# Performance work log

Hardware: AMD Instinct MI355X
Metric: run time of the kernel (lower is better)

The kernel has to match this reference:

```python
import jax, jax.numpy as jnp
import numpy as np

NUM_EXPERT = 64
TOP_K = 2
N_TOKENS = 16384
H_DIM = 4096


def setup_inputs() -> dict:
    key = jax.random.key(0)
    k1, k2, k3 = jax.random.split(key, 3)
    x = jax.random.normal(k1, (N_TOKENS, H_DIM), dtype=jnp.float32)
    # nn.Linear(h_dim, num_expert): weight [E, H], bias [E]
    W = jax.random.normal(k2, (NUM_EXPERT, H_DIM), dtype=jnp.float32) * (1.0 / np.sqrt(H_DIM))
    b = jax.random.normal(k3, (NUM_EXPERT,), dtype=jnp.float32) * 0.01
    return {"x": x, "W": W, "b": b}


def reference(x, W, b):
    # gating linear: [N, H] @ [H, E] + [E] -> [N, E]
    router_logits = x @ W.T + b
    # softmax over experts in float32 (matches dtype=torch.float)
    router_probs = jax.nn.softmax(router_logits.astype(jnp.float32), axis=1)
    # top-k over experts (values sorted descending, like torch.topk)
    router_weights, selected_experts_idx = jax.lax.top_k(router_probs, TOP_K)
    # renormalize via second softmax over the top_k dim (dim=1 of [N, K])
    router_weights = jax.nn.softmax(router_weights, axis=1).astype(x.dtype)
    # one-hot expert mask [N, K, E] -> permute(2,1,0) -> [E, K, N]
    expert_mask = jax.nn.one_hot(selected_experts_idx, NUM_EXPERT, dtype=jnp.int32)
    expert_mask = jnp.transpose(expert_mask, (2, 1, 0))
    return router_logits, router_weights, selected_experts_idx, expert_mask
```

## Files before the change

### kernel.cpp

```cpp
#include <hip/hip_runtime.h>
#include <hip/hip_bf16.h>
#include <math.h>

#define H_DIM 4096
#define N_EXP 64
#define N_TOK 16384
#define BM    32
#define KB    64
#define NCHUNK (H_DIM / KB)
#define MARGIN 1e-3f
#define SLOT_BYTES 24576

typedef __attribute__((ext_vector_type(8))) short short8v;
typedef __attribute__((ext_vector_type(4))) float float4v;

__device__ __forceinline__ unsigned short bf16_rn(float f) {
    unsigned u = __builtin_bit_cast(unsigned, f);
    u += 0x7FFFu + ((u >> 16) & 1u);
    return (unsigned short)(u >> 16);
}
__device__ __forceinline__ float bf16_hi_f32(unsigned u) {
    return __builtin_bit_cast(float, u & 0xFFFF0000u);
}
__device__ __forceinline__ void gload_lds16(const void* g, void* l) {
    __builtin_amdgcn_global_load_lds(
        (const __attribute__((address_space(1))) unsigned int*)g,
        (__attribute__((address_space(3))) unsigned int*)l, 16, 0, 0);
}

__global__ __launch_bounds__(256)
void wconvert_kernel(const float* __restrict__ W,
                     unsigned short* __restrict__ wh,
                     unsigned short* __restrict__ wm,
                     int* __restrict__ counter) {
    int i = blockIdx.x * 256 + threadIdx.x;
    if (i == 0) *counter = 0;
    float w = W[i];
    unsigned u = __builtin_bit_cast(unsigned, w);
    wh[i] = (unsigned short)(u >> 16);
    wm[i] = bf16_rn(w - bf16_hi_f32(u));
}

__global__ __launch_bounds__(512, 4)
void router_mfma_kernel(const float* __restrict__ x,
                        const unsigned short* __restrict__ wh,
                        const unsigned short* __restrict__ wm,
                        const float* __restrict__ bias,
                        float* __restrict__ logits,
                        float* __restrict__ wout,
                        float* __restrict__ iout,
                        int* __restrict__ counter,
                        int* __restrict__ list) {
    __shared__ char smem[2 * SLOT_BYTES];
    float* olds = (float*)smem;

    const int tid  = threadIdx.x;
    const int lane = tid & 63;
    const int wid  = __builtin_amdgcn_readfirstlane(tid >> 6);
    const int tok0 = blockIdx.x * BM;

    const int q    = lane >> 4;
    const int e15  = lane & 15;
    const int mt   = wid & 1;
    const int eg   = wid >> 1;
    const int arow = mt * 16 + e15;
    const int er   = eg * 16 + e15;

    float4v acc = {0.f, 0.f, 0.f, 0.f};

    auto stage = [&](int slot, int kc) {
        char* base = smem + slot * SLOT_BYTES;
        {
            int row = tid >> 4, u = tid & 15;
            int us  = u ^ (row & 15);
            const float* src = x + (size_t)(tok0 + row) * H_DIM + kc + us * 4;
            gload_lds16(src, base + (size_t)(wid * 64) * 16);
        }
#pragma unroll
        for (int j = 0; j < 2; ++j) {
            int idx = j * 512 + tid;
            int s = idx >> 9, e = (idx >> 3) & 63, u = idx & 7;
            int us = u ^ (e & 7);
            const unsigned short* wsrc = s ? wm : wh;
            const unsigned short* src  = wsrc + (size_t)e * H_DIM + kc + us * 8;
            gload_lds16(src, base + 8192 + (size_t)(j * 512 + wid * 64) * 16);
        }
    };

    auto compute = [&](int slot) {
        const char* xc = smem + slot * SLOT_BYTES;
        const char* wc = xc + 8192;
#pragma unroll
        for (int t = 0; t < 2; ++t) {
            float f[8];
#pragma unroll
            for (int h = 0; h < 2; ++h) {
                int u = (t * 8 + q * 2 + h) ^ (arow & 15);
                float4 a = *(const float4*)(xc + (size_t)(arow * 16 + u) * 16);
                f[h * 4 + 0] = a.x; f[h * 4 + 1] = a.y;
                f[h * 4 + 2] = a.z; f[h * 4 + 3] = a.w;
            }
            short8v ah, am;
#pragma unroll
            for (int j = 0; j < 8; ++j) {
                unsigned u = __builtin_bit_cast(unsigned, f[j]);
                ah[j] = (short)(u >> 16);
                am[j] = (short)bf16_rn(f[j] - bf16_hi_f32(u));
            }
            int up = (t * 4 + q) ^ (e15 & 7);
            short8v bh = *(const short8v*)(wc + (size_t)(er * 8 + up) * 16);
            short8v bm = *(const short8v*)(wc + 8192 + (size_t)(er * 8 + up) * 16);

            acc = __builtin_amdgcn_mfma_f32_16x16x32_bf16(ah, bh, acc, 0, 0, 0);
            acc = __builtin_amdgcn_mfma_f32_16x16x32_bf16(am, bh, acc, 0, 0, 0);
            acc = __builtin_amdgcn_mfma_f32_16x16x32_bf16(ah, bm, acc, 0, 0, 0);
            acc = __builtin_amdgcn_mfma_f32_16x16x32_bf16(am, bm, acc, 0, 0, 0);
        }
    };

    stage(0, 0);
    for (int c = 0; c < NCHUNK; ++c) {
        __builtin_amdgcn_s_barrier();
        if (c + 1 < NCHUNK) {
            stage((c + 1) & 1, (c + 1) * KB);
            asm volatile("s_waitcnt vmcnt(3)" ::: "memory");
        } else {
            asm volatile("s_waitcnt vmcnt(0)" ::: "memory");
        }
        __builtin_amdgcn_s_barrier();
        compute(c & 1);
    }
    __syncthreads();

    float bv = bias[er];
#pragma unroll
    for (int r = 0; r < 4; ++r) {
        int trow = mt * 16 + q * 4 + r;
        float v = acc[r] + bv;
        logits[(size_t)(tok0 + trow) * N_EXP + er] = v;
        olds[trow * 66 + er] = v;
    }
    __syncthreads();

#pragma unroll
    for (int it = 0; it < 4; ++it) {
        const int nl = wid * 4 + it;
        const int n  = tok0 + nl;
        float l = olds[nl * 66 + lane];

        float v1 = l; int i1 = lane;
#pragma unroll
        for (int off = 32; off >= 1; off >>= 1) {
            float ov = __shfl_xor(v1, off);
            int   oi = __shfl_xor(i1, off);
            if (ov > v1 || (ov == v1 && oi < i1)) { v1 = ov; i1 = oi; }
        }
        float l2 = (lane == i1) ? -INFINITY : l;
        float v2 = l2; int i2 = lane;
#pragma unroll
        for (int off = 32; off >= 1; off >>= 1) {
            float ov = __shfl_xor(v2, off);
            int   oi = __shfl_xor(i2, off);
            if (ov > v2 || (ov == v2 && oi < i2)) { v2 = ov; i2 = oi; }
        }
        float l3 = (lane == i1 || lane == i2) ? -INFINITY : l;
        float v3 = l3;
#pragma unroll
        for (int off = 32; off >= 1; off >>= 1)
            v3 = fmaxf(v3, __shfl_xor(v3, off));

        float Z = expf(l - v1);
#pragma unroll
        for (int off = 32; off >= 1; off >>= 1) Z += __shfl_xor(Z, off);

        if (lane == 0) {
            float p1 = 1.0f / Z;
            float p2 = expf(v2 - v1) / Z;
            float t  = expf(p2 - p1);
            wout[2 * n + 0] = 1.0f / (1.0f + t);
            wout[2 * n + 1] = t / (1.0f + t);
            iout[2 * n + 0] = (float)i1;
            iout[2 * n + 1] = (float)i2;
            if ((v1 - v2 < MARGIN) || (v2 - v3 < MARGIN)) {
                int sidx = atomicAdd(counter, 1);
                list[sidx] = n;
            }
        }
    }
}

__global__ __launch_bounds__(256)
void router_logits_f32(const float* __restrict__ x,
                       const float* __restrict__ W,
                       const float* __restrict__ bias,
                       float* __restrict__ logits) {
    __shared__ float4 wlds[32 * 64];
    __shared__ float4 xlds[32][32];
    const int tid = threadIdx.x;
    const int lane = tid & 63;
    const int wid = __builtin_amdgcn_readfirstlane(tid >> 6);
    const int tok0b = blockIdx.x * 32;
    const int trow0 = wid * 8;
    float acc[8];
#pragma unroll
    for (int t = 0; t < 8; ++t) acc[t] = 0.0f;
    for (int kc = 0; kc < H_DIM; kc += 128) {
        __syncthreads();
#pragma unroll
        for (int i = 0; i < 8; ++i) {
            int idx = tid + i * 256;
            int se = idx >> 5, sj = idx & 31;
            float4 v = *(const float4*)(W + (size_t)se * H_DIM + kc + sj * 4);
            wlds[sj * 64 + (se ^ (sj & 7))] = v;
        }
#pragma unroll
        for (int i = 0; i < 4; ++i) {
            int idx = tid + i * 256;
            int row = idx >> 5, col = idx & 31;
            xlds[row][col] = *(const float4*)(x + (size_t)(tok0b + row) * H_DIM + kc + col * 4);
        }
        __syncthreads();
#pragma unroll 4
        for (int jg = 0; jg < 32; ++jg) {
            float4 w = wlds[jg * 64 + (lane ^ (jg & 7))];
#pragma unroll
            for (int t = 0; t < 8; ++t) {
                float4 xv = xlds[trow0 + t][jg];
                acc[t] = fmaf(w.x, xv.x, acc[t]);
                acc[t] = fmaf(w.y, xv.y, acc[t]);
                acc[t] = fmaf(w.z, xv.z, acc[t]);
                acc[t] = fmaf(w.w, xv.w, acc[t]);
            }
        }
    }
    float bv = bias[lane];
#pragma unroll
    for (int t = 0; t < 8; ++t)
        logits[(size_t)(tok0b + trow0 + t) * N_EXP + lane] = acc[t] + bv;
}

__global__ __launch_bounds__(256)
void topk_kernel(const float* __restrict__ logits,
                 float* __restrict__ wout,
                 float* __restrict__ iout) {
    const int lane = threadIdx.x & 63;
    const int wid  = threadIdx.x >> 6;
    const int wg   = blockIdx.x * 4 + wid;
#pragma unroll
    for (int it = 0; it < 4; ++it) {
        const int n = wg * 4 + it;
        float l = logits[(size_t)n * N_EXP + lane];
        float v1 = l; int i1 = lane;
#pragma unroll
        for (int off = 32; off >= 1; off >>= 1) {
            float ov = __shfl_xor(v1, off);
            int   oi = __shfl_xor(i1, off);
            if (ov > v1 || (ov == v1 && oi < i1)) { v1 = ov; i1 = oi; }
        }
        float l2 = (lane == i1) ? -INFINITY : l;
        float v2 = l2; int i2 = lane;
#pragma unroll
        for (int off = 32; off >= 1; off >>= 1) {
            float ov = __shfl_xor(v2, off);
            int   oi = __shfl_xor(i2, off);
            if (ov > v2 || (ov == v2 && oi < i2)) { v2 = ov; i2 = oi; }
        }
        float Z = expf(l - v1);
#pragma unroll
        for (int off = 32; off >= 1; off >>= 1) Z += __shfl_xor(Z, off);
        if (lane == 0) {
            float p1 = 1.0f / Z;
            float p2 = expf(v2 - v1) / Z;
            float t  = expf(p2 - p1);
            wout[2 * n + 0] = 1.0f / (1.0f + t);
            wout[2 * n + 1] = t / (1.0f + t);
            iout[2 * n + 0] = (float)i1;
            iout[2 * n + 1] = (float)i2;
        }
    }
}

__global__ __launch_bounds__(256)
void fixup_kernel(const float* __restrict__ x,
                  const float* __restrict__ W,
                  const float* __restrict__ bias,
                  float* __restrict__ wout,
                  float* __restrict__ iout,
                  const int* __restrict__ counter,
                  const int* __restrict__ list) {
    __shared__ float plds[4][64];
    __shared__ float llds[64];
    int cnt = counter[0];
    if (cnt > N_TOK) cnt = N_TOK;
    const int e = threadIdx.x & 63;
    const int s = threadIdx.x >> 6;
    for (int it = blockIdx.x; it < cnt; it += 128) {
        int n = list[it];
        const float4* xr = (const float4*)(x + (size_t)n * H_DIM) + s * 256;
        const float4* wr = (const float4*)(W + (size_t)e * H_DIM) + s * 256;
        float p = 0.f;
#pragma unroll 8
        for (int j = 0; j < 256; ++j) {
            float4 a = xr[j], w = wr[j];
            p = fmaf(a.x, w.x, p); p = fmaf(a.y, w.y, p);
            p = fmaf(a.z, w.z, p); p = fmaf(a.w, w.w, p);
        }
        plds[s][e] = p;
        __syncthreads();
        if (threadIdx.x < 64)
            llds[e] = ((plds[0][e] + plds[1][e]) + (plds[2][e] + plds[3][e])) + bias[e];
        __syncthreads();
        if (threadIdx.x == 0) {
            float v1 = -INFINITY, v2 = -INFINITY;
            int i1 = 0, i2 = 0;
            for (int i = 0; i < 64; ++i) {
                float li = llds[i];
                if (li > v1)      { v2 = v1; i2 = i1; v1 = li; i1 = i; }
                else if (li > v2) { v2 = li; i2 = i; }
            }
            float Z = 0.0f;
            for (int i = 0; i < 64; ++i) Z += expf(llds[i] - v1);
            float p1 = 1.0f / Z;
            float p2 = expf(v2 - v1) / Z;
            float t  = expf(p2 - p1);
            wout[2 * n + 0] = 1.0f / (1.0f + t);
            wout[2 * n + 1] = t / (1.0f + t);
            iout[2 * n + 0] = (float)i1;
            iout[2 * n + 1] = (float)i2;
        }
        __syncthreads();
    }
}

__global__ __launch_bounds__(256)
void mask_kernel(const float* __restrict__ iout,
                 float* __restrict__ mask) {
    int gid = blockIdx.x * 256 + threadIdx.x;
    int n   = gid & (N_TOK - 1);
    int ek  = gid >> 14;
    float idxf = iout[(size_t)n * 2 + (ek & 1)];
    mask[gid] = (idxf == (float)(ek >> 1)) ? 1.0f : 0.0f;
}

extern "C" void kernel_launch(void* const* d_in, const int* in_sizes, int n_in,
                              void* d_out, int out_size, void* d_ws, size_t ws_size,
                              hipStream_t stream) {
    const float* x  = (const float*)d_in[0];
    const float* W  = (const float*)d_in[1];
    const float* b  = (const float*)d_in[2];

    float* out    = (float*)d_out;
    float* logits = out;
    float* wout   = logits + (size_t)N_TOK * 64;
    float* iout   = wout   + (size_t)N_TOK * 2;
    float* mask   = iout   + (size_t)N_TOK * 2;

    const size_t wsplit = (size_t)N_EXP * H_DIM;
    const size_t need   = 2 * wsplit * sizeof(unsigned short) + 4 + (size_t)N_TOK * 4;
    if (ws_size >= need) {
        unsigned short* wh = (unsigned short*)d_ws;
        unsigned short* wm = wh + wsplit;
        int* counter = (int*)((char*)d_ws + 2 * wsplit * sizeof(unsigned short));
        int* list    = counter + 1;
        wconvert_kernel<<<(int)(wsplit / 256), 256, 0, stream>>>(W, wh, wm, counter);
        router_mfma_kernel<<<N_TOK / BM, 512, 0, stream>>>(x, wh, wm, b, logits,
                                                           wout, iout, counter, list);
        fixup_kernel<<<128, 256, 0, stream>>>(x, W, b, wout, iout, counter, list);
    } else {
        router_logits_f32<<<N_TOK / 32, 256, 0, stream>>>(x, W, b, logits);
        topk_kernel<<<N_TOK / 16, 256, 0, stream>>>(logits, wout, iout);
    }
    mask_kernel<<<(N_EXP * 2 * N_TOK) / 256, 256, 0, stream>>>(iout, mask);
}
```

Measured before the change: 148.5 us.

## Replace LDS-staged GEMM with split-K direct global loads and LDS reduction

The router GEMM kernel drops its double-buffered LDS staging through global_load_lds. Blocks are now 16 tokens by 4 waves, and each wave covers a quarter of the K dimension for all 64 experts, loading x and the bf16 weight halves straight from global memory into registers with a one-step prefetch of x. Partial sums are reduced in LDS before the bias, logits store and top-k stage. This removes the per-chunk barriers and LDS traffic but depends on L2/cache reuse of the weights across the many more blocks, and the direct loads are less coalesced.

```diff
diff --git a/kernel.cpp b/kernel.cpp
--- a/kernel.cpp
+++ b/kernel.cpp
@@ -5,11 +5,11 @@
 #define H_DIM 4096
 #define N_EXP 64
 #define N_TOK 16384
-#define BM    32
-#define KB    64
-#define NCHUNK (H_DIM / KB)
+#define BM    16
+#define NKS   4
+#define KSL   (H_DIM / NKS)
+#define NSTEP (KSL / 32)
 #define MARGIN 1e-3f
-#define SLOT_BYTES 24576
 
 typedef __attribute__((ext_vector_type(8))) short short8v;
 typedef __attribute__((ext_vector_type(4))) float float4v;
@@ -21,11 +21,6 @@
 }
 __device__ __forceinline__ float bf16_hi_f32(unsigned u) {
     return __builtin_bit_cast(float, u & 0xFFFF0000u);
-}
-__device__ __forceinline__ void gload_lds16(const void* g, void* l) {
-    __builtin_amdgcn_global_load_lds(
-        (const __attribute__((address_space(1))) unsigned int*)g,
-        (__attribute__((address_space(3))) unsigned int*)l, 16, 0, 0);
 }
 
 __global__ __launch_bounds__(256)
@@ -41,7 +36,7 @@
     wm[i] = bf16_rn(w - bf16_hi_f32(u));
 }
 
-__global__ __launch_bounds__(512, 4)
+__global__ __launch_bounds__(256, 4)
 void router_mfma_kernel(const float* __restrict__ x,
                         const unsigned short* __restrict__ wh,
                         const unsigned short* __restrict__ wm,
@@ -51,94 +46,91 @@
                         float* __restrict__ iout,
                         int* __restrict__ counter,
                         int* __restrict__ list) {
-    __shared__ char smem[2 * SLOT_BYTES];
-    float* olds = (float*)smem;
+    __shared__ float part[NKS][16][66];
+    __shared__ float olds[16][66];
 
     const int tid  = threadIdx.x;
     const int lane = tid & 63;
     const int wid  = __builtin_amdgcn_readfirstlane(tid >> 6);
     const int tok0 = blockIdx.x * BM;
 
-    const int q    = lane >> 4;
-    const int e15  = lane & 15;
-    const int mt   = wid & 1;
-    const int eg   = wid >> 1;
-    const int arow = mt * 16 + e15;
-    const int er   = eg * 16 + e15;
-
-    float4v acc = {0.f, 0.f, 0.f, 0.f};
-
-    auto stage = [&](int slot, int kc) {
-        char* base = smem + slot * SLOT_BYTES;
-        {
-            int row = tid >> 4, u = tid & 15;
-            int us  = u ^ (row & 15);
-            const float* src = x + (size_t)(tok0 + row) * H_DIM + kc + us * 4;
-            gload_lds16(src, base + (size_t)(wid * 64) * 16);
-        }
-#pragma unroll
-        for (int j = 0; j < 2; ++j) {
-            int idx = j * 512 + tid;
-            int s = idx >> 9, e = (idx >> 3) & 63, u = idx & 7;
-            int us = u ^ (e & 7);
-            const unsigned short* wsrc = s ? wm : wh;
-            const unsigned short* src  = wsrc + (size_t)e * H_DIM + kc + us * 8;
-            gload_lds16(src, base + 8192 + (size_t)(j * 512 + wid * 64) * 16);
-        }
-    };
-
-    auto compute = [&](int slot) {
-        const char* xc = smem + slot * SLOT_BYTES;
-        const char* wc = xc + 8192;
-#pragma unroll
-        for (int t = 0; t < 2; ++t) {
-            float f[8];
-#pragma unroll
-            for (int h = 0; h < 2; ++h) {
-                int u = (t * 8 + q * 2 + h) ^ (arow & 15);
-                float4 a = *(const float4*)(xc + (size_t)(arow * 16 + u) * 16);
-                f[h * 4 + 0] = a.x; f[h * 4 + 1] = a.y;
-                f[h * 4 + 2] = a.z; f[h * 4 + 3] = a.w;
-            }
-            short8v ah, am;
-#pragma unroll
-            for (int j = 0; j < 8; ++j) {
-                unsigned u = __builtin_bit_cast(unsigned, f[j]);
-                ah[j] = (short)(u >> 16);
-                am[j] = (short)bf16_rn(f[j] - bf16_hi_f32(u));
-            }
-            int up = (t * 4 + q) ^ (e15 & 7);
-            short8v bh = *(const short8v*)(wc + (size_t)(er * 8 + up) * 16);
-            short8v bm = *(const short8v*)(wc + 8192 + (size_t)(er * 8 + up) * 16);
-
-            acc = __builtin_amdgcn_mfma_f32_16x16x32_bf16(ah, bh, acc, 0, 0, 0);
-            acc = __builtin_amdgcn_mfma_f32_16x16x32_bf16(am, bh, acc, 0, 0, 0);
-            acc = __builtin_amdgcn_mfma_f32_16x16x32_bf16(ah, bm, acc, 0, 0, 0);
-            acc = __builtin_amdgcn_mfma_f32_16x16x32_bf16(am, bm, acc, 0, 0, 0);
-        }
-    };
-
-    stage(0, 0);
-    for (int c = 0; c < NCHUNK; ++c) {
-        __builtin_amdgcn_s_barrier();
-        if (c + 1 < NCHUNK) {
-            stage((c + 1) & 1, (c + 1) * KB);
-            asm volatile("s_waitcnt vmcnt(3)" ::: "memory");
-        } else {
-            asm volatile("s_waitcnt vmcnt(0)" ::: "memory");
-        }
-        __builtin_amdgcn_s_barrier();
-        compute(c & 1);
+    const int q     = lane >> 4;
+    const int e15   = lane & 15;
+    const int kbase = wid * KSL;
+
+    const float* xp = x + (size_t)(tok0 + e15) * H_DIM + kbase + q * 8;
+    const unsigned short* whp = wh + (size_t)e15 * H_DIM + kbase + q * 8;
+    const unsigned short* wmp = wm + (size_t)e15 * H_DIM + kbase + q * 8;
+
+    float4v acc0 = {0.f,0.f,0.f,0.f}, acc1 = {0.f,0.f,0.f,0.f};
+    float4v acc2 = {0.f,0.f,0.f,0.f}, acc3 = {0.f,0.f,0.f,0.f};
+
+    float4 a0 = *(const float4*)(xp);
+    float4 a1 = *(const float4*)(xp + 4);
+
+    for (int s = 0; s < NSTEP; ++s) {
+        float4 n0, n1;
+        if (s + 1 < NSTEP) {
+            const float* nxt = xp + (size_t)(s + 1) * 32;
+            n0 = *(const float4*)(nxt);
+            n1 = *(const float4*)(nxt + 4);
+        } else { n0 = a0; n1 = a1; }
+
+        float f[8] = {a0.x,a0.y,a0.z,a0.w,a1.x,a1.y,a1.z,a1.w};
+        short8v ah, am;
+#pragma unroll
+        for (int j = 0; j < 8; ++j) {
+            unsigned u = __builtin_bit_cast(unsigned, f[j]);
+            ah[j] = (short)(u >> 16);
+            am[j] = (short)bf16_rn(f[j] - bf16_hi_f32(u));
+        }
+
+        const size_t ko = (size_t)s * 32;
+        {   short8v bh = *(const short8v*)(whp + ko);
+            short8v bm = *(const short8v*)(wmp + ko);
+            acc0 = __builtin_amdgcn_mfma_f32_16x16x32_bf16(ah, bh, acc0, 0, 0, 0);
+            acc0 = __builtin_amdgcn_mfma_f32_16x16x32_bf16(am, bh, acc0, 0, 0, 0);
+            acc0 = __builtin_amdgcn_mfma_f32_16x16x32_bf16(ah, bm, acc0, 0, 0, 0);
+            acc0 = __builtin_amdgcn_mfma_f32_16x16x32_bf16(am, bm, acc0, 0, 0, 0); }
+        {   short8v bh = *(const short8v*)(whp + (size_t)16 * H_DIM + ko);
+            short8v bm = *(const short8v*)(wmp + (size_t)16 * H_DIM + ko);
+            acc1 = __builtin_amdgcn_mfma_f32_16x16x32_bf16(ah, bh, acc1, 0, 0, 0);
+            acc1 = __builtin_amdgcn_mfma_f32_16x16x32_bf16(am, bh, acc1, 0, 0, 0);
+            acc1 = __builtin_amdgcn_mfma_f32_16x16x32_bf16(ah, bm, acc1, 0, 0, 0);
+            acc1 = __builtin_amdgcn_mfma_f32_16x16x32_bf16(am, bm, acc1, 0, 0, 0); }
+        {   short8v bh = *(const short8v*)(whp + (size_t)32 * H_DIM + ko);
+            short8v bm = *(const short8v*)(wmp + (size_t)32 * H_DIM + ko);
+            acc2 = __builtin_amdgcn_mfma_f32_16x16x32_bf16(ah, bh, acc2, 0, 0, 0);
+            acc2 = __builtin_amdgcn_mfma_f32_16x16x32_bf16(am, bh, acc2, 0, 0, 0);
+            acc2 = __builtin_amdgcn_mfma_f32_16x16x32_bf16(ah, bm, acc2, 0, 0, 0);
+            acc2 = __builtin_amdgcn_mfma_f32_16x16x32_bf16(am, bm, acc2, 0, 0, 0); }
+        {   short8v bh = *(const short8v*)(whp + (size_t)48 * H_DIM + ko);
+            short8v bm = *(const short8v*)(wmp + (size_t)48 * H_DIM + ko);
+            acc3 = __builtin_amdgcn_mfma_f32_16x16x32_bf16(ah, bh, acc3, 0, 0, 0);
+            acc3 = __builtin_amdgcn_mfma_f32_16x16x32_bf16(am, bh, acc3, 0, 0, 0);
+            acc3 = __builtin_amdgcn_mfma_f32_16x16x32_bf16(ah, bm, acc3, 0, 0, 0);
+            acc3 = __builtin_amdgcn_mfma_f32_16x16x32_bf16(am, bm, acc3, 0, 0, 0); }
+
+        a0 = n0; a1 = n1;
+    }
+
+#pragma unroll
+    for (int r = 0; r < 4; ++r) {
+        part[wid][q * 4 + r][ 0 + e15] = acc0[r];
+        part[wid][q * 4 + r][16 + e15] = acc1[r];
+        part[wid][q * 4 + r][32 + e15] = acc2[r];
+        part[wid][q * 4 + r][48 + e15] = acc3[r];
     }
     __syncthreads();
 
-    float bv = bias[er];
-#pragma unroll
-    for (int r = 0; r < 4; ++r) {
-        int trow = mt * 16 + q * 4 + r;
-        float v = acc[r] + bv;
-        logits[(size_t)(tok0 + trow) * N_EXP + er] = v;
-        olds[trow * 66 + er] = v;
+#pragma unroll
+    for (int i = 0; i < 4; ++i) {
+        int o  = i * 256 + tid;
+        int tk = o >> 6, e = o & 63;
+        float v = ((part[0][tk][e] + part[1][tk][e]) +
+                   (part[2][tk][e] + part[3][tk][e])) + bias[e];
+        logits[(size_t)(tok0 + tk) * N_EXP + e] = v;
+        olds[tk][e] = v;
     }
     __syncthreads();
 
@@ -146,7 +138,7 @@
     for (int it = 0; it < 4; ++it) {
         const int nl = wid * 4 + it;
         const int n  = tok0 + nl;
-        float l = olds[nl * 66 + lane];
+        float l = olds[nl][lane];
 
         float v1 = l; int i1 = lane;
 #pragma unroll
@@ -363,7 +355,7 @@
         int* counter = (int*)((char*)d_ws + 2 * wsplit * sizeof(unsigned short));
         int* list    = counter + 1;
         wconvert_kernel<<<(int)(wsplit / 256), 256, 0, stream>>>(W, wh, wm, counter);
-        router_mfma_kernel<<<N_TOK / BM, 512, 0, stream>>>(x, wh, wm, b, logits,
+        router_mfma_kernel<<<N_TOK / BM, 256, 0, stream>>>(x, wh, wm, b, logits,
                                                            wout, iout, counter, list);
         fixup_kernel<<<128, 256, 0, stream>>>(x, W, b, wout, iout, counter, list);
     } else {
```

After: 226.6 us. 1.53x slower.
